# Kernel optimization log

Measured on AMD Instinct MI355X. Metric: run time of the kernel, lower is better.

Reference implementation:

```python
import jax, jax.numpy as jnp
import numpy as np

B, S, D = 2, 2048, 1024
H, KVH, HD = 16, 4, 64
ROPE_THETA = 10000.0


def rotate_half(x):
    h = x.shape[-1] // 2
    return jnp.concatenate([-x[..., h:], x[..., :h]], axis=-1)


def setup_inputs() -> dict:
    key = jax.random.key(0)
    k = jax.random.split(key, 6)
    x = jax.random.normal(k[0], (B, S, D), dtype=jnp.float32)
    # real RoPE tables: [S, HD//2]
    inv_freq = 1.0 / (ROPE_THETA ** (jnp.arange(0, HD, 2, dtype=jnp.float32) / HD))
    t = jnp.arange(S, dtype=jnp.float32)
    freqs = jnp.outer(t, inv_freq)  # [S, HD/2]
    cos = jnp.cos(freqs)
    sin = jnp.sin(freqs)
    # causal additive mask [1,1,S,S]
    neg = jnp.float32(-1e9)
    mask = jnp.where(jnp.tril(jnp.ones((S, S), dtype=bool)), 0.0, neg)[None, None]
    scale = 0.02
    wq = jax.random.normal(k[1], (D, H * HD), dtype=jnp.float32) * scale
    wk = jax.random.normal(k[2], (D, KVH * HD), dtype=jnp.float32) * scale
    wv = jax.random.normal(k[3], (D, KVH * HD), dtype=jnp.float32) * scale
    wo = jax.random.normal(k[4], (H * HD, D), dtype=jnp.float32) * scale
    return {"x": x, "cos": cos, "sin": sin, "mask": mask,
            "wq": wq, "wk": wk, "wv": wv, "wo": wo}


def reference(x, cos, sin, mask, wq, wk, wv, wo):
    b, s, d = x.shape
    hd = 2 * cos.shape[-1]
    h = wq.shape[1] // hd
    kvh = wk.shape[1] // hd
    n_rep = h // kvh

    q = (x @ wq).reshape(b, s, h, hd)
    k = (x @ wk).reshape(b, s, kvh, hd)
    v = (x @ wv).reshape(b, s, kvh, hd)

    # RoPE: cos/sin [S, hd/2] -> [1, s, 1, hd] via self-concat (rotate_half style)
    c = jnp.concatenate([cos[:s], cos[:s]], axis=-1)[None, :, None, :]
    sn = jnp.concatenate([sin[:s], sin[:s]], axis=-1)[None, :, None, :]
    q = q * c + rotate_half(q) * sn
    k = k * c + rotate_half(k) * sn

    new_k, new_v = k, v  # kv cache (pre-repeat)

    # GQA: repeat each kv head n_rep times contiguously (== expand+reshape)
    if n_rep > 1:
        k = jnp.repeat(k, n_rep, axis=2)
        v = jnp.repeat(v, n_rep, axis=2)

    scores = jnp.einsum('bqhd,bkhd->bhqk', q, k) / jnp.sqrt(jnp.float32(hd))
    scores = scores + mask
    attn = jax.nn.softmax(scores.astype(jnp.float32), axis=-1).astype(q.dtype)
    out = jnp.einsum('bhqk,bkhd->bqhd', attn, v).reshape(b, s, h * hd)
    out = out @ wo
    return (out, new_k, new_v)
```

## Files before the change

### kernel.cpp

```cpp
#include <hip/hip_runtime.h>
#include <hip/hip_bf16.h>

constexpr int B_ = 2, S_ = 2048, D_ = 1024, H_ = 16, KVH_ = 4, HD_ = 64;

typedef __attribute__((ext_vector_type(8))) short short8;
typedef __attribute__((ext_vector_type(4))) float f32x4;
typedef __attribute__((ext_vector_type(16))) float f32x16;

__device__ inline short f2b(float x) {
  unsigned u = __float_as_uint(x);
  return (short)((u + 0x7fffu + ((u >> 16) & 1u)) >> 16);
}
__device__ inline unsigned pkbf2(float lo, float hi) {
  __hip_bfloat162 h = __float22bfloat162_rn(float2{lo, hi});
  return *(unsigned*)&h;
}

__device__ inline void async16(void* lds, const void* g) {
  __builtin_amdgcn_global_load_lds(
      (const __attribute__((address_space(1))) unsigned int*)g,
      (__attribute__((address_space(3))) unsigned int*)lds, 16, 0, 0);
}

__global__ __launch_bounds__(256) void prep_kernel(
    const float* __restrict__ x, short* __restrict__ xb,
    const float* __restrict__ wq, const float* __restrict__ wk,
    const float* __restrict__ wv, const float* __restrict__ wo,
    short* __restrict__ wt, short* __restrict__ wot) {
  __shared__ short ts[64][66];
  const int tid = threadIdx.x;
  if (blockIdx.x < 4096) {
    const int idx = (blockIdx.x * 256 + tid) * 4;
    float4 v = *(const float4*)(x + idx);
    short4 o;
    o.x = f2b(v.x); o.y = f2b(v.y); o.z = f2b(v.z); o.w = f2b(v.w);
    *(short4*)(xb + idx) = o;
    return;
  }
  const int bid = blockIdx.x - 4096;
  const int z = bid >> 8, bi = (bid >> 4) & 15, bj = bid & 15;
  const float* W;
  short* dst;
  int N;
  if (z == 0)      { W = wq; dst = wt;                       N = 1024; }
  else if (z == 1) { W = wo; dst = wot;                      N = 1024; }
  else if (z == 2) { W = wk; dst = wt + (size_t)1024 * 1024; N = 256; }
  else             { W = wv; dst = wt + (size_t)1280 * 1024; N = 256; }
  if (bj * 64 >= N) return;
#pragma unroll
  for (int i = 0; i < 16; ++i) {
    int idx = tid + i * 256;
    int r = idx >> 6, c = idx & 63;
    ts[r][c] = f2b(W[(size_t)(bi * 64 + r) * N + bj * 64 + c]);
  }
  __syncthreads();
#pragma unroll
  for (int i = 0; i < 16; ++i) {
    int idx = tid + i * 256;
    int cc = idx >> 6, rr = idx & 63;
    dst[(size_t)(bj * 64 + cc) * 1024 + bi * 64 + rr] = ts[rr][cc];
  }
}

struct GemmLds64 {
  short As[2][64][32];
  short Bs[2][128][32];
};

__device__ inline void gemm_core64(GemmLds64& lds, const short* __restrict__ A,
                                   const short* __restrict__ Bt, int K,
                                   int row0, int col0, int tid,
                                   f32x4 (&acc)[8]) {
  const int w = tid >> 6, lane = tid & 63;
  const int grp = lane >> 4, li = lane & 15;
#pragma unroll
  for (int nt = 0; nt < 8; ++nt) acc[nt] = (f32x4){0.f, 0.f, 0.f, 0.f};

  auto issue = [&](int bi, int k0) {
    async16((short*)&lds.As[bi][0][0] + tid * 8,
            A + (size_t)(row0 + (tid >> 2)) * K + k0 + (tid & 3) * 8);
#pragma unroll
    for (int i = 0; i < 2; ++i) {
      const int idx = i * 256 + tid;
      async16((short*)&lds.Bs[bi][0][0] + idx * 8,
              Bt + (size_t)(col0 + (idx >> 2)) * K + k0 + (idx & 3) * 8);
    }
  };

  issue(0, 0);
  const int nk = K >> 5;
  for (int kk = 0; kk < nk; ++kk) {
    const int cur = kk & 1;
    __syncthreads();
    if (kk + 1 < nk) issue(cur ^ 1, (kk + 1) << 5);

    const short8 af = *(const short8*)&lds.As[cur][w * 16 + li][grp * 8];
    short8 bf[8];
#pragma unroll
    for (int nt = 0; nt < 8; ++nt)
      bf[nt] = *(const short8*)&lds.Bs[cur][nt * 16 + li][grp * 8];
#pragma unroll
    for (int nt = 0; nt < 8; ++nt)
      acc[nt] = __builtin_amdgcn_mfma_f32_16x16x32_bf16(af, bf[nt], acc[nt],
                                                        0, 0, 0);
  }
}

#define QSCALE 0.1803368801111f

__global__ __launch_bounds__(256) void gemm_qkv(
    const short* __restrict__ A, const short* __restrict__ Bt,
    const float* __restrict__ cs, const float* __restrict__ sn,
    short* __restrict__ qb, float* __restrict__ koutp, short* __restrict__ kb,
    float* __restrict__ voutp, short* __restrict__ vbT) {
  __shared__ GemmLds64 lds;
  const int tid = threadIdx.x;
  const int w = tid >> 6, lane = tid & 63;
  const int grp = lane >> 4, li = lane & 15;
  const int row0 = blockIdx.y * 64, col0 = blockIdx.x * 128;
  f32x4 acc[8];
  gemm_core64(lds, A, Bt, D_, row0, col0, tid, acc);

  if (col0 < 1024) {
#pragma unroll
    for (int h2 = 0; h2 < 2; ++h2)
#pragma unroll
      for (int p = 0; p < 2; ++p) {
        const int nt = h2 * 4 + p;
#pragma unroll
        for (int r = 0; r < 4; ++r) {
          const int row = row0 + w * 16 + grp * 4 + r;
          const int spos = row & (S_ - 1);
          const int col = col0 + nt * 16 + li;
          const int d = p * 16 + li;
          const float c = cs[spos * 32 + d];
          const float s = sn[spos * 32 + d];
          const float x0 = acc[nt][r], x1 = acc[nt + 2][r];
          qb[(size_t)row * 1024 + col] = f2b((x0 * c - x1 * s) * QSCALE);
          qb[(size_t)row * 1024 + col + 32] = f2b((x1 * c + x0 * s) * QSCALE);
        }
      }
  } else if (col0 < 1280) {
#pragma unroll
    for (int h2 = 0; h2 < 2; ++h2)
#pragma unroll
      for (int p = 0; p < 2; ++p) {
        const int nt = h2 * 4 + p;
#pragma unroll
        for (int r = 0; r < 4; ++r) {
          const int row = row0 + w * 16 + grp * 4 + r;
          const int bq = row >> 11, spos = row & (S_ - 1);
          const int sb = spos >> 5, k32 = spos & 31;
          const int kcol = col0 + nt * 16 + li - 1024;
          const int khk = kcol >> 6, d = kcol & 63;
          const float c = cs[spos * 32 + d];
          const float s = sn[spos * 32 + d];
          const float x0 = acc[nt][r], x1 = acc[nt + 2][r];
          const float k0v = x0 * c - x1 * s;
          const float k1v = x1 * c + x0 * s;
          koutp[(size_t)row * 256 + kcol] = k0v;
          koutp[(size_t)row * 256 + kcol + 32] = k1v;
          short* kbase =
              kb + (((size_t)(bq * 4 + khk) * 64 + sb) * 2048) + k32 * 8;
          const int d2 = d + 32;
          kbase[((d >> 4) * 2 + ((d >> 3) & 1)) * 256 + (d & 7)] = f2b(k0v);
          kbase[((d2 >> 4) * 2 + ((d2 >> 3) & 1)) * 256 + (d2 & 7)] = f2b(k1v);
        }
      }
  } else {
#pragma unroll
    for (int nt = 0; nt < 8; ++nt) {
      const int vcol = col0 + nt * 16 + li - 1280;
      const int row_base = row0 + w * 16 + grp * 4;
      short4 pk;
      float vv[4];
#pragma unroll
      for (int r = 0; r < 4; ++r) vv[r] = acc[nt][r];
      pk.x = f2b(vv[0]); pk.y = f2b(vv[1]);
      pk.z = f2b(vv[2]); pk.w = f2b(vv[3]);
#pragma unroll
      for (int r = 0; r < 4; ++r)
        voutp[(size_t)(row_base + r) * 256 + vcol] = vv[r];
      const int bq = row_base >> 11, s0 = row_base & (S_ - 1);
      const int t = s0 >> 6, k64 = s0 & 63;
      const int kc = k64 >> 4, kg8 = (k64 >> 3) & 1, k8 = k64 & 7;
      const int khv = vcol >> 6, d = vcol & 63;
      short* vb = vbT + (((size_t)(bq * 4 + khv) * 32 + t) * 4096) +
                  (d >> 5) * 2048 + kc * 512 + kg8 * 256 + (d & 31) * 8 + k8;
      *(short4*)vb = pk;
    }
  }
}

__global__ __launch_bounds__(128) void fattn_kernel(
    const short* __restrict__ qb, const short* __restrict__ kb,
    const short* __restrict__ vbT, short* __restrict__ o) {
  __shared__ float scr[64 * 33 + 32];

  const int tid = threadIdx.x;
  const int par = tid >> 6, lane = tid & 63;
  const int n32 = lane & 31, kg = lane >> 5;

  const int qt = 63 - (blockIdx.x >> 5);
  const int bh = blockIdx.x & 31;
  const int b = bh >> 4, h = bh & 15, kh = h >> 2;
  const int qq = qt >> 1, st = qt & 1;
  const int nt = qq + 1;

  const short* qp =
      qb + ((size_t)(b * S_ + qt * 32 + n32)) * 1024 + h * 64 + kg * 8;
  short8 qa[4];
#pragma unroll
  for (int ks = 0; ks < 4; ++ks) qa[ks] = *(const short8*)(qp + ks * 16);

  const short* kF = kb + ((size_t)(b * 4 + kh) << 17) + lane * 8;
  const short* vF = vbT + ((size_t)(b * 4 + kh) << 17) + lane * 8;

  f32x16 zero16;
#pragma unroll
  for (int i = 0; i < 16; ++i) zero16[i] = 0.f;
  f32x16 Oa0 = zero16, Oa1 = zero16;
  float lreg = 0.f;

  auto loadK = [&](int t, short8 (&kr)[8]) {
    const short* kt = kF + (size_t)t * 4096;
#pragma unroll
    for (int s = 0; s < 2; ++s)
#pragma unroll
      for (int ks = 0; ks < 4; ++ks)
        kr[s * 4 + ks] = *(const short8*)(kt + s * 2048 + ks * 512);
  };
  auto loadV = [&](int t, short8 (&vr)[8]) {
    const short* vt = vF + (size_t)t * 4096;
#pragma unroll
    for (int kc = 0; kc < 4; ++kc) {
      vr[kc] = *(const short8*)(vt + kc * 512);
      vr[kc + 4] = *(const short8*)(vt + 2048 + kc * 512);
    }
  };

  auto body = [&](int t, const short8 (&kr)[8], const short8 (&vr)[8]) {
    const bool diag = (t == qq);
    unsigned pk[4][4];
#pragma unroll
    for (int s = 0; s < 2; ++s) {
      if (s == 1 && diag && st == 0) continue;
      __builtin_amdgcn_s_setprio(1);
      f32x16 sv = __builtin_amdgcn_mfma_f32_32x32x16_bf16(kr[s * 4 + 0], qa[0],
                                                          zero16, 0, 0, 0);
      sv = __builtin_amdgcn_mfma_f32_32x32x16_bf16(kr[s * 4 + 1], qa[1], sv, 0,
                                                   0, 0);
      sv = __builtin_amdgcn_mfma_f32_32x32x16_bf16(kr[s * 4 + 2], qa[2], sv, 0,
                                                   0, 0);
      sv = __builtin_amdgcn_mfma_f32_32x32x16_bf16(kr[s * 4 + 3], qa[3], sv, 0,
                                                   0, 0);
      __builtin_amdgcn_s_setprio(0);
      const bool dm = diag && (s == st);
      float e[16];
#pragma unroll
      for (int rr = 0; rr < 16; ++rr) {
        float v = __builtin_amdgcn_exp2f(sv[rr]);
        if (dm) {
          const int key32 = (rr & 3) + 8 * (rr >> 2) + 4 * kg;
          if (key32 > n32) v = 0.f;
        }
        e[rr] = v;
      }
      pk[2 * s][0] = pkbf2(e[0], e[1]);
      pk[2 * s][1] = pkbf2(e[2], e[3]);
      pk[2 * s][2] = pkbf2(e[4], e[5]);
      pk[2 * s][3] = pkbf2(e[6], e[7]);
      pk[2 * s + 1][0] = pkbf2(e[8], e[9]);
      pk[2 * s + 1][1] = pkbf2(e[10], e[11]);
      pk[2 * s + 1][2] = pkbf2(e[12], e[13]);
      pk[2 * s + 1][3] = pkbf2(e[14], e[15]);
      lreg += (((e[0] + e[1]) + (e[2] + e[3])) +
               ((e[4] + e[5]) + (e[6] + e[7]))) +
              (((e[8] + e[9]) + (e[10] + e[11])) +
               ((e[12] + e[13]) + (e[14] + e[15])));
    }

    auto pv = [&](int kc) {
      auto r02 =
          __builtin_amdgcn_permlane32_swap(pk[kc][0], pk[kc][2], false, false);
      auto r13 =
          __builtin_amdgcn_permlane32_swap(pk[kc][1], pk[kc][3], false, false);
      union { unsigned u[4]; short8 s8; } f;
      f.u[0] = r02[0]; f.u[1] = r13[0]; f.u[2] = r02[1]; f.u[3] = r13[1];
      Oa0 = __builtin_amdgcn_mfma_f32_32x32x16_bf16(vr[kc], f.s8, Oa0, 0, 0, 0);
      Oa1 = __builtin_amdgcn_mfma_f32_32x32x16_bf16(vr[kc + 4], f.s8, Oa1, 0,
                                                    0, 0);
    };
    __builtin_amdgcn_s_setprio(1);
    if (diag && st == 0) {
      pv(0); pv(1);
    } else {
      pv(0); pv(1); pv(2); pv(3);
    }
    __builtin_amdgcn_s_setprio(0);
  };

  {
    short8 kA[8], kB[8], vA[8], vB[8];
    int t = par;
    if (t < nt) {
      loadK(t, kA);
      loadV(t, vA);
      for (;;) {
        if (t + 2 < nt) { loadV(t + 2, vB); loadK(t + 2, kB); }
        body(t, kA, vA);
        t += 2;
        if (t >= nt) break;
        if (t + 2 < nt) { loadV(t + 2, vA); loadK(t + 2, kA); }
        body(t, kB, vB);
        t += 2;
        if (t >= nt) break;
      }
    }
  }

  lreg += __shfl_xor(lreg, 32);

  float* lb = scr + 64 * 33;
  if (par == 1) {
#pragma unroll
    for (int rr = 0; rr < 16; ++rr) {
      const int d0 = (rr & 3) + 8 * (rr >> 2) + 4 * kg;
      scr[d0 * 33 + n32] = Oa0[rr];
      scr[(d0 + 32) * 33 + n32] = Oa1[rr];
    }
    if (kg == 0) lb[n32] = lreg;
  }
  __syncthreads();
  if (par == 0) {
    const float inv = __builtin_amdgcn_rcpf(lreg + lb[n32]);
#pragma unroll
    for (int rr = 0; rr < 16; ++rr) {
      const int d0 = (rr & 3) + 8 * (rr >> 2) + 4 * kg;
      scr[d0 * 33 + n32] = (Oa0[rr] + scr[d0 * 33 + n32]) * inv;
      scr[(d0 + 32) * 33 + n32] = (Oa1[rr] + scr[(d0 + 32) * 33 + n32]) * inv;
    }
  }
  __syncthreads();
  {
    const int q = tid >> 2, seg = (tid & 3) * 16;
    const size_t gb = ((size_t)(b * S_ + qt * 32 + q)) * 1024 + h * 64 + seg;
    short8 t0, t1;
#pragma unroll
    for (int k2 = 0; k2 < 8; ++k2) {
      t0[k2] = f2b(scr[(seg + k2) * 33 + q]);
      t1[k2] = f2b(scr[(seg + 8 + k2) * 33 + q]);
    }
    *(short8*)(o + gb) = t0;
    *(short8*)(o + gb + 8) = t1;
  }
}

__global__ __launch_bounds__(256) void gemm_bt_f32(
    const short* __restrict__ A, const short* __restrict__ Bt,
    float* __restrict__ C, int N, int K) {
  __shared__ GemmLds64 lds;
  const int tid = threadIdx.x;
  const int w = tid >> 6, lane = tid & 63;
  const int grp = lane >> 4, li = lane & 15;
  const int row0 = blockIdx.y * 64, col0 = blockIdx.x * 128;
  f32x4 acc[8];
  gemm_core64(lds, A, Bt, K, row0, col0, tid, acc);
#pragma unroll
  for (int nt = 0; nt < 8; ++nt)
#pragma unroll
    for (int r = 0; r < 4; ++r)
      C[(size_t)(row0 + w * 16 + grp * 4 + r) * N + col0 + nt * 16 + li] =
          acc[nt][r];
}

extern "C" void kernel_launch(void* const* d_in, const int* in_sizes, int n_in,
                              void* d_out, int out_size, void* d_ws,
                              size_t ws_size, hipStream_t stream) {
  const float* x  = (const float*)d_in[0];
  const float* cs = (const float*)d_in[1];
  const float* sn = (const float*)d_in[2];
  const float* wq = (const float*)d_in[4];
  const float* wk = (const float*)d_in[5];
  const float* wv = (const float*)d_in[6];
  const float* wo = (const float*)d_in[7];

  float* outp  = (float*)d_out;
  float* koutp = outp + (size_t)B_ * S_ * H_ * HD_;
  float* voutp = koutp + (size_t)B_ * S_ * KVH_ * HD_;

  char* p = (char*)d_ws;
  short* xb   = (short*)p; p += (size_t)B_ * S_ * D_ * 2;
  short* qb   = (short*)p; p += (size_t)B_ * S_ * H_ * HD_ * 2;
  short* kb   = (short*)p; p += (size_t)B_ * S_ * KVH_ * HD_ * 2;
  short* vbT  = (short*)p; p += (size_t)B_ * S_ * KVH_ * HD_ * 2;
  short* abuf = (short*)p; p += (size_t)B_ * S_ * H_ * HD_ * 2;
  short* wt   = (short*)p; p += (size_t)1536 * D_ * 2;
  short* wot  = (short*)p; p += (size_t)D_ * H_ * HD_ * 2;

  const int M = B_ * S_;

  prep_kernel<<<4096 + 1024, 256, 0, stream>>>(x, xb, wq, wk, wv, wo, wt,
                                               wot);

  gemm_qkv<<<dim3(1536 / 128, M / 64), 256, 0, stream>>>(
      xb, wt, cs, sn, qb, koutp, kb, voutp, vbT);

  fattn_kernel<<<64 * 32, 128, 0, stream>>>(qb, kb, vbT, abuf);

  gemm_bt_f32<<<dim3(1024 / 128, M / 64), 256, 0, stream>>>(abuf, wot, outp,
                                                            1024, 1024);
}
```

Before: 172.0 us.

## Share K/V tiles via double-buffered LDS across 64-query attention blocks

The attention kernel now processes 64 queries per block with 4 waves instead of 32 queries with 2 waves. Each 64-key K/V tile is loaded cooperatively into a double-buffered LDS array, and the two query halves read it from there. Before, each wave streamed K/V from global memory into registers on its own. Blocks are halved and global K/V traffic per query drops, at the cost of a __syncthreads per tile and LDS reads. The key-split across waves also changes from alternating tiles to splitting each tile into halves.

```diff
diff --git a/kernel.cpp b/kernel.cpp
--- a/kernel.cpp
+++ b/kernel.cpp
@@ -192,29 +192,30 @@
   }
 }
 
-__global__ __launch_bounds__(128) void fattn_kernel(
+__global__ __launch_bounds__(256) void fattn_kernel(
     const short* __restrict__ qb, const short* __restrict__ kb,
     const short* __restrict__ vbT, short* __restrict__ o) {
-  __shared__ float scr[64 * 33 + 32];
+  __shared__ short kv[2][8192];
 
   const int tid = threadIdx.x;
-  const int par = tid >> 6, lane = tid & 63;
+  const int w = tid >> 6, lane = tid & 63;
   const int n32 = lane & 31, kg = lane >> 5;
-
-  const int qt = 63 - (blockIdx.x >> 5);
+  const int qhalf = w & 1, ks2 = w >> 1;
+
+  const int qt = 31 - (blockIdx.x >> 5);
   const int bh = blockIdx.x & 31;
   const int b = bh >> 4, h = bh & 15, kh = h >> 2;
-  const int qq = qt >> 1, st = qt & 1;
-  const int nt = qq + 1;
+  const int nt = qt + 1;
 
   const short* qp =
-      qb + ((size_t)(b * S_ + qt * 32 + n32)) * 1024 + h * 64 + kg * 8;
+      qb + ((size_t)(b * S_ + qt * 64 + qhalf * 32 + n32)) * 1024 + h * 64 +
+      kg * 8;
   short8 qa[4];
 #pragma unroll
   for (int ks = 0; ks < 4; ++ks) qa[ks] = *(const short8*)(qp + ks * 16);
 
-  const short* kF = kb + ((size_t)(b * 4 + kh) << 17) + lane * 8;
-  const short* vF = vbT + ((size_t)(b * 4 + kh) << 17) + lane * 8;
+  const short* kF = kb + ((size_t)(b * 4 + kh) << 17);
+  const short* vF = vbT + ((size_t)(b * 4 + kh) << 17);
 
   f32x16 zero16;
 #pragma unroll
@@ -222,134 +223,125 @@
   f32x16 Oa0 = zero16, Oa1 = zero16;
   float lreg = 0.f;
 
-  auto loadK = [&](int t, short8 (&kr)[8]) {
-    const short* kt = kF + (size_t)t * 4096;
-#pragma unroll
-    for (int s = 0; s < 2; ++s)
-#pragma unroll
-      for (int ks = 0; ks < 4; ++ks)
-        kr[s * 4 + ks] = *(const short8*)(kt + s * 2048 + ks * 512);
+  short8 st0, st1, st2, st3;
+  auto gload = [&](int t) {
+    const short* gk = kF + (size_t)t * 4096;
+    const short* gv = vF + (size_t)t * 4096;
+    st0 = *(const short8*)(gk + tid * 8);
+    st1 = *(const short8*)(gk + 2048 + tid * 8);
+    st2 = *(const short8*)(gv + tid * 8);
+    st3 = *(const short8*)(gv + 2048 + tid * 8);
   };
-  auto loadV = [&](int t, short8 (&vr)[8]) {
-    const short* vt = vF + (size_t)t * 4096;
-#pragma unroll
-    for (int kc = 0; kc < 4; ++kc) {
-      vr[kc] = *(const short8*)(vt + kc * 512);
-      vr[kc + 4] = *(const short8*)(vt + 2048 + kc * 512);
-    }
+  auto swrite = [&](int bi) {
+    *(short8*)&kv[bi][tid * 8] = st0;
+    *(short8*)&kv[bi][2048 + tid * 8] = st1;
+    *(short8*)&kv[bi][4096 + tid * 8] = st2;
+    *(short8*)&kv[bi][6144 + tid * 8] = st3;
   };
 
-  auto body = [&](int t, const short8 (&kr)[8], const short8 (&vr)[8]) {
-    const bool diag = (t == qq);
-    unsigned pk[4][4];
-#pragma unroll
-    for (int s = 0; s < 2; ++s) {
-      if (s == 1 && diag && st == 0) continue;
-      __builtin_amdgcn_s_setprio(1);
-      f32x16 sv = __builtin_amdgcn_mfma_f32_32x32x16_bf16(kr[s * 4 + 0], qa[0],
-                                                          zero16, 0, 0, 0);
-      sv = __builtin_amdgcn_mfma_f32_32x32x16_bf16(kr[s * 4 + 1], qa[1], sv, 0,
-                                                   0, 0);
-      sv = __builtin_amdgcn_mfma_f32_32x32x16_bf16(kr[s * 4 + 2], qa[2], sv, 0,
-                                                   0, 0);
-      sv = __builtin_amdgcn_mfma_f32_32x32x16_bf16(kr[s * 4 + 3], qa[3], sv, 0,
-                                                   0, 0);
-      __builtin_amdgcn_s_setprio(0);
-      const bool dm = diag && (s == st);
-      float e[16];
-#pragma unroll
-      for (int rr = 0; rr < 16; ++rr) {
-        float v = __builtin_amdgcn_exp2f(sv[rr]);
-        if (dm) {
-          const int key32 = (rr & 3) + 8 * (rr >> 2) + 4 * kg;
-          if (key32 > n32) v = 0.f;
-        }
-        e[rr] = v;
+  auto compute = [&](int t, int cur) {
+    const bool diag = (t == qt);
+    if (diag && ks2 > qhalf) return;
+
+    short8 kf[4];
+#pragma unroll
+    for (int ks = 0; ks < 4; ++ks)
+      kf[ks] = *(const short8*)&kv[cur][ks2 * 2048 + ks * 512 + lane * 8];
+    __builtin_amdgcn_s_setprio(1);
+    f32x16 sv =
+        __builtin_amdgcn_mfma_f32_32x32x16_bf16(kf[0], qa[0], zero16, 0, 0, 0);
+    sv = __builtin_amdgcn_mfma_f32_32x32x16_bf16(kf[1], qa[1], sv, 0, 0, 0);
+    sv = __builtin_amdgcn_mfma_f32_32x32x16_bf16(kf[2], qa[2], sv, 0, 0, 0);
+    sv = __builtin_amdgcn_mfma_f32_32x32x16_bf16(kf[3], qa[3], sv, 0, 0, 0);
+    __builtin_amdgcn_s_setprio(0);
+
+    const bool dm = diag && (ks2 == qhalf);
+    float e[16];
+#pragma unroll
+    for (int rr = 0; rr < 16; ++rr) {
+      float v = __builtin_amdgcn_exp2f(sv[rr]);
+      if (dm) {
+        const int key32 = (rr & 3) + 8 * (rr >> 2) + 4 * kg;
+        if (key32 > n32) v = 0.f;
       }
-      pk[2 * s][0] = pkbf2(e[0], e[1]);
-      pk[2 * s][1] = pkbf2(e[2], e[3]);
-      pk[2 * s][2] = pkbf2(e[4], e[5]);
-      pk[2 * s][3] = pkbf2(e[6], e[7]);
-      pk[2 * s + 1][0] = pkbf2(e[8], e[9]);
-      pk[2 * s + 1][1] = pkbf2(e[10], e[11]);
-      pk[2 * s + 1][2] = pkbf2(e[12], e[13]);
-      pk[2 * s + 1][3] = pkbf2(e[14], e[15]);
-      lreg += (((e[0] + e[1]) + (e[2] + e[3])) +
-               ((e[4] + e[5]) + (e[6] + e[7]))) +
-              (((e[8] + e[9]) + (e[10] + e[11])) +
-               ((e[12] + e[13]) + (e[14] + e[15])));
-    }
-
-    auto pv = [&](int kc) {
+      e[rr] = v;
+    }
+    unsigned pk[2][4];
+    pk[0][0] = pkbf2(e[0], e[1]);
+    pk[0][1] = pkbf2(e[2], e[3]);
+    pk[0][2] = pkbf2(e[4], e[5]);
+    pk[0][3] = pkbf2(e[6], e[7]);
+    pk[1][0] = pkbf2(e[8], e[9]);
+    pk[1][1] = pkbf2(e[10], e[11]);
+    pk[1][2] = pkbf2(e[12], e[13]);
+    pk[1][3] = pkbf2(e[14], e[15]);
+    lreg += (((e[0] + e[1]) + (e[2] + e[3])) + ((e[4] + e[5]) + (e[6] + e[7]))) +
+            (((e[8] + e[9]) + (e[10] + e[11])) +
+             ((e[12] + e[13]) + (e[14] + e[15])));
+
+    __builtin_amdgcn_s_setprio(1);
+#pragma unroll
+    for (int j = 0; j < 2; ++j) {
+      const int kc = ks2 * 2 + j;
       auto r02 =
-          __builtin_amdgcn_permlane32_swap(pk[kc][0], pk[kc][2], false, false);
+          __builtin_amdgcn_permlane32_swap(pk[j][0], pk[j][2], false, false);
       auto r13 =
-          __builtin_amdgcn_permlane32_swap(pk[kc][1], pk[kc][3], false, false);
+          __builtin_amdgcn_permlane32_swap(pk[j][1], pk[j][3], false, false);
       union { unsigned u[4]; short8 s8; } f;
       f.u[0] = r02[0]; f.u[1] = r13[0]; f.u[2] = r02[1]; f.u[3] = r13[1];
-      Oa0 = __builtin_amdgcn_mfma_f32_32x32x16_bf16(vr[kc], f.s8, Oa0, 0, 0, 0);
-      Oa1 = __builtin_amdgcn_mfma_f32_32x32x16_bf16(vr[kc + 4], f.s8, Oa1, 0,
-                                                    0, 0);
-    };
-    __builtin_amdgcn_s_setprio(1);
-    if (diag && st == 0) {
-      pv(0); pv(1);
-    } else {
-      pv(0); pv(1); pv(2); pv(3);
+      const short8 v0 = *(const short8*)&kv[cur][4096 + kc * 512 + lane * 8];
+      const short8 v1 = *(const short8*)&kv[cur][6144 + kc * 512 + lane * 8];
+      Oa0 = __builtin_amdgcn_mfma_f32_32x32x16_bf16(v0, f.s8, Oa0, 0, 0, 0);
+      Oa1 = __builtin_amdgcn_mfma_f32_32x32x16_bf16(v1, f.s8, Oa1, 0, 0, 0);
     }
     __builtin_amdgcn_s_setprio(0);
   };
 
-  {
-    short8 kA[8], kB[8], vA[8], vB[8];
-    int t = par;
-    if (t < nt) {
-      loadK(t, kA);
-      loadV(t, vA);
-      for (;;) {
-        if (t + 2 < nt) { loadV(t + 2, vB); loadK(t + 2, kB); }
-        body(t, kA, vA);
-        t += 2;
-        if (t >= nt) break;
-        if (t + 2 < nt) { loadV(t + 2, vA); loadK(t + 2, kA); }
-        body(t, kB, vB);
-        t += 2;
-        if (t >= nt) break;
-      }
-    }
+  gload(0);
+  swrite(0);
+  for (int t = 0; t < nt; ++t) {
+    const int cur = t & 1;
+    __syncthreads();
+    if (t + 1 < nt) gload(t + 1);
+    compute(t, cur);
+    if (t + 1 < nt) swrite(cur ^ 1);
   }
 
   lreg += __shfl_xor(lreg, 32);
 
-  float* lb = scr + 64 * 33;
-  if (par == 1) {
+  __syncthreads();
+  float* scr = (float*)&kv[0][0];
+  float* lb = scr + 64 * 65;
+  const int qcol = qhalf * 32 + n32;
+  if (ks2 == 1) {
 #pragma unroll
     for (int rr = 0; rr < 16; ++rr) {
       const int d0 = (rr & 3) + 8 * (rr >> 2) + 4 * kg;
-      scr[d0 * 33 + n32] = Oa0[rr];
-      scr[(d0 + 32) * 33 + n32] = Oa1[rr];
-    }
-    if (kg == 0) lb[n32] = lreg;
+      scr[d0 * 65 + qcol] = Oa0[rr];
+      scr[(d0 + 32) * 65 + qcol] = Oa1[rr];
+    }
+    if (kg == 0) lb[qcol] = lreg;
   }
   __syncthreads();
-  if (par == 0) {
-    const float inv = __builtin_amdgcn_rcpf(lreg + lb[n32]);
+  if (ks2 == 0) {
+    const float inv = __builtin_amdgcn_rcpf(lreg + lb[qcol]);
 #pragma unroll
     for (int rr = 0; rr < 16; ++rr) {
       const int d0 = (rr & 3) + 8 * (rr >> 2) + 4 * kg;
-      scr[d0 * 33 + n32] = (Oa0[rr] + scr[d0 * 33 + n32]) * inv;
-      scr[(d0 + 32) * 33 + n32] = (Oa1[rr] + scr[(d0 + 32) * 33 + n32]) * inv;
+      scr[d0 * 65 + qcol] = (Oa0[rr] + scr[d0 * 65 + qcol]) * inv;
+      scr[(d0 + 32) * 65 + qcol] =
+          (Oa1[rr] + scr[(d0 + 32) * 65 + qcol]) * inv;
     }
   }
   __syncthreads();
   {
     const int q = tid >> 2, seg = (tid & 3) * 16;
-    const size_t gb = ((size_t)(b * S_ + qt * 32 + q)) * 1024 + h * 64 + seg;
+    const size_t gb = ((size_t)(b * S_ + qt * 64 + q)) * 1024 + h * 64 + seg;
     short8 t0, t1;
 #pragma unroll
     for (int k2 = 0; k2 < 8; ++k2) {
-      t0[k2] = f2b(scr[(seg + k2) * 33 + q]);
-      t1[k2] = f2b(scr[(seg + 8 + k2) * 33 + q]);
+      t0[k2] = f2b(scr[(seg + k2) * 65 + q]);
+      t1[k2] = f2b(scr[(seg + 8 + k2) * 65 + q]);
     }
     *(short8*)(o + gb) = t0;
     *(short8*)(o + gb + 8) = t1;
@@ -406,7 +398,7 @@
   gemm_qkv<<<dim3(1536 / 128, M / 64), 256, 0, stream>>>(
       xb, wt, cs, sn, qb, koutp, kb, voutp, vbT);
 
-  fattn_kernel<<<64 * 32, 128, 0, stream>>>(qb, kb, vbT, abuf);
+  fattn_kernel<<<32 * 32, 256, 0, stream>>>(qb, kb, vbT, abuf);
 
   gemm_bt_f32<<<dim3(1024 / 128, M / 64), 256, 0, stream>>>(abuf, wot, outp,
                                                             1024, 1024);
```

After: 178.6 us. 1.04x slower.

## Pre-tile GEMM operands into MFMA fragment order for contiguous loads

Applied to the files above, without the earlier changes.

Producers (prep kernel for x and weights, attention output writer) now store A and B operands in a blocked layout matching the per-wave MFMA fragment order: 64x32 A tiles and 128x32 B tiles, each contiguous. The GEMM core then does fully contiguous 16-byte async copies and conflict-free linear LDS reads instead of strided row loads and row-indexed LDS reads. This removes strided global access and LDS bank conflicts, at the cost of scattered writes in the producers and a layout tied to fixed tile sizes.

```diff
diff --git a/kernel.cpp b/kernel.cpp
--- a/kernel.cpp
+++ b/kernel.cpp
@@ -21,6 +21,7 @@
       (const __attribute__((address_space(1))) unsigned int*)g,
       (__attribute__((address_space(3))) unsigned int*)lds, 16, 0, 0);
 }
+
 
 __global__ __launch_bounds__(256) void prep_kernel(
     const float* __restrict__ x, short* __restrict__ xb,
@@ -34,18 +35,22 @@
     float4 v = *(const float4*)(x + idx);
     short4 o;
     o.x = f2b(v.x); o.y = f2b(v.y); o.z = f2b(v.z); o.w = f2b(v.w);
-    *(short4*)(xb + idx) = o;
+    const int row = idx >> 10, k = idx & 1023;
+    const int rb = row >> 6, w16 = (row >> 4) & 3, li = row & 15;
+    const int kb = k >> 5, grp = (k >> 3) & 3, e0 = k & 7;
+    *(short4*)(xb + ((size_t)(rb * 32 + kb)) * 2048 + w16 * 512 +
+               (grp * 16 + li) * 8 + e0) = o;
     return;
   }
   const int bid = blockIdx.x - 4096;
   const int z = bid >> 8, bi = (bid >> 4) & 15, bj = bid & 15;
   const float* W;
   short* dst;
-  int N;
-  if (z == 0)      { W = wq; dst = wt;                       N = 1024; }
-  else if (z == 1) { W = wo; dst = wot;                      N = 1024; }
-  else if (z == 2) { W = wk; dst = wt + (size_t)1024 * 1024; N = 256; }
-  else             { W = wv; dst = wt + (size_t)1280 * 1024; N = 256; }
+  int N, colbase;
+  if (z == 0)      { W = wq; dst = wt;  N = 1024; colbase = 0; }
+  else if (z == 1) { W = wo; dst = wot; N = 1024; colbase = 0; }
+  else if (z == 2) { W = wk; dst = wt;  N = 256;  colbase = 1024; }
+  else             { W = wv; dst = wt;  N = 256;  colbase = 1280; }
   if (bj * 64 >= N) return;
 #pragma unroll
   for (int i = 0; i < 16; ++i) {
@@ -58,47 +63,47 @@
   for (int i = 0; i < 16; ++i) {
     int idx = tid + i * 256;
     int cc = idx >> 6, rr = idx & 63;
-    dst[(size_t)(bj * 64 + cc) * 1024 + bi * 64 + rr] = ts[rr][cc];
+    const int colg = colbase + bj * 64 + cc;
+    const int k = bi * 64 + rr;
+    const int cb2 = colg >> 7, nt2 = (colg >> 4) & 7, li2 = colg & 15;
+    const int kb2 = k >> 5, grp2 = (k >> 3) & 3, e2 = k & 7;
+    dst[((size_t)(cb2 * 32 + kb2)) * 4096 + nt2 * 512 + (grp2 * 16 + li2) * 8 +
+        e2] = ts[rr][cc];
   }
 }
 
 struct GemmLds64 {
-  short As[2][64][32];
-  short Bs[2][128][32];
+  short As[2][2048];
+  short Bs[2][4096];
 };
 
-__device__ inline void gemm_core64(GemmLds64& lds, const short* __restrict__ A,
-                                   const short* __restrict__ Bt, int K,
-                                   int row0, int col0, int tid,
-                                   f32x4 (&acc)[8]) {
+__device__ inline void gemm_core64f(GemmLds64& lds, const short* __restrict__ Af,
+                                    const short* __restrict__ Bf, int nkb,
+                                    int rb, int cb, int tid,
+                                    f32x4 (&acc)[8]) {
   const int w = tid >> 6, lane = tid & 63;
-  const int grp = lane >> 4, li = lane & 15;
 #pragma unroll
   for (int nt = 0; nt < 8; ++nt) acc[nt] = (f32x4){0.f, 0.f, 0.f, 0.f};
 
-  auto issue = [&](int bi, int k0) {
-    async16((short*)&lds.As[bi][0][0] + tid * 8,
-            A + (size_t)(row0 + (tid >> 2)) * K + k0 + (tid & 3) * 8);
-#pragma unroll
-    for (int i = 0; i < 2; ++i) {
-      const int idx = i * 256 + tid;
-      async16((short*)&lds.Bs[bi][0][0] + idx * 8,
-              Bt + (size_t)(col0 + (idx >> 2)) * K + k0 + (idx & 3) * 8);
-    }
+  auto issue = [&](int bi, int kb) {
+    const short* a = Af + ((size_t)(rb * nkb + kb)) * 2048;
+    const short* b = Bf + ((size_t)(cb * nkb + kb)) * 4096;
+    async16(&lds.As[bi][tid * 8], a + tid * 8);
+    async16(&lds.Bs[bi][tid * 8], b + tid * 8);
+    async16(&lds.Bs[bi][2048 + tid * 8], b + 2048 + tid * 8);
   };
 
   issue(0, 0);
-  const int nk = K >> 5;
-  for (int kk = 0; kk < nk; ++kk) {
+  for (int kk = 0; kk < nkb; ++kk) {
     const int cur = kk & 1;
     __syncthreads();
-    if (kk + 1 < nk) issue(cur ^ 1, (kk + 1) << 5);
-
-    const short8 af = *(const short8*)&lds.As[cur][w * 16 + li][grp * 8];
+    if (kk + 1 < nkb) issue(cur ^ 1, kk + 1);
+
+    const short8 af = *(const short8*)&lds.As[cur][w * 512 + lane * 8];
     short8 bf[8];
 #pragma unroll
     for (int nt = 0; nt < 8; ++nt)
-      bf[nt] = *(const short8*)&lds.Bs[cur][nt * 16 + li][grp * 8];
+      bf[nt] = *(const short8*)&lds.Bs[cur][nt * 512 + lane * 8];
 #pragma unroll
     for (int nt = 0; nt < 8; ++nt)
       acc[nt] = __builtin_amdgcn_mfma_f32_16x16x32_bf16(af, bf[nt], acc[nt],
@@ -117,9 +122,10 @@
   const int tid = threadIdx.x;
   const int w = tid >> 6, lane = tid & 63;
   const int grp = lane >> 4, li = lane & 15;
-  const int row0 = blockIdx.y * 64, col0 = blockIdx.x * 128;
+  const int rb = blockIdx.y, cb = blockIdx.x;
+  const int row0 = rb * 64, col0 = cb * 128;
   f32x4 acc[8];
-  gemm_core64(lds, A, Bt, D_, row0, col0, tid, acc);
+  gemm_core64f(lds, A, Bt, 32, rb, cb, tid, acc);
 
   if (col0 < 1024) {
 #pragma unroll
@@ -344,28 +350,33 @@
   __syncthreads();
   {
     const int q = tid >> 2, seg = (tid & 3) * 16;
-    const size_t gb = ((size_t)(b * S_ + qt * 32 + q)) * 1024 + h * 64 + seg;
+    const int row = b * S_ + qt * 32 + q;
+    const int rb = row >> 6, w16 = (row >> 4) & 3, li = row & 15;
     short8 t0, t1;
 #pragma unroll
     for (int k2 = 0; k2 < 8; ++k2) {
       t0[k2] = f2b(scr[(seg + k2) * 33 + q]);
       t1[k2] = f2b(scr[(seg + 8 + k2) * 33 + q]);
     }
-    *(short8*)(o + gb) = t0;
-    *(short8*)(o + gb + 8) = t1;
+    const int c0 = h * 64 + seg, c1 = c0 + 8;
+    *(short8*)(o + ((size_t)(rb * 32 + (c0 >> 5))) * 2048 + w16 * 512 +
+               (((c0 >> 3) & 3) * 16 + li) * 8) = t0;
+    *(short8*)(o + ((size_t)(rb * 32 + (c1 >> 5))) * 2048 + w16 * 512 +
+               (((c1 >> 3) & 3) * 16 + li) * 8) = t1;
   }
 }
 
 __global__ __launch_bounds__(256) void gemm_bt_f32(
     const short* __restrict__ A, const short* __restrict__ Bt,
-    float* __restrict__ C, int N, int K) {
+    float* __restrict__ C, int N, int nkb) {
   __shared__ GemmLds64 lds;
   const int tid = threadIdx.x;
   const int w = tid >> 6, lane = tid & 63;
   const int grp = lane >> 4, li = lane & 15;
-  const int row0 = blockIdx.y * 64, col0 = blockIdx.x * 128;
+  const int rb = blockIdx.y, cb = blockIdx.x;
   f32x4 acc[8];
-  gemm_core64(lds, A, Bt, K, row0, col0, tid, acc);
+  gemm_core64f(lds, A, Bt, nkb, rb, cb, tid, acc);
+  const int row0 = rb * 64, col0 = cb * 128;
 #pragma unroll
   for (int nt = 0; nt < 8; ++nt)
 #pragma unroll
@@ -403,11 +414,10 @@
   prep_kernel<<<4096 + 1024, 256, 0, stream>>>(x, xb, wq, wk, wv, wo, wt,
                                                wot);
 
-  gemm_qkv<<<dim3(1536 / 128, M / 64), 256, 0, stream>>>(
+  gemm_qkv<<<dim3(12, M / 64), 256, 0, stream>>>(
       xb, wt, cs, sn, qb, koutp, kb, voutp, vbT);
 
   fattn_kernel<<<64 * 32, 128, 0, stream>>>(qb, kb, vbT, abuf);
 
-  gemm_bt_f32<<<dim3(1024 / 128, M / 64), 256, 0, stream>>>(abuf, wot, outp,
-                                                            1024, 1024);
-}
+  gemm_bt_f32<<<dim3(8, M / 64), 256, 0, stream>>>(abuf, wot, outp, 1024, 32);
+}
```

After: 174.2 us. No clear change (+1.3%).
